# Optimization experiments

Hardware: AMD Instinct MI355X
Metric: run time of the kernel (lower is better)

## Reference

```python
import jax, jax.numpy as jnp
import numpy as np

NUM_GRAPHS = 64
EPS = 1e-5


def _bn(x, g, b):
    # training-mode BatchNorm1d with biased variance (as torch uses for normalization)
    m = x.mean(axis=0)
    v = x.var(axis=0)
    return (x - m) * jax.lax.rsqrt(v + EPS) * g + b


def setup_inputs() -> dict:
    key = jax.random.key(0)
    ks = jax.random.split(key, 16)
    N, E, F, T, H = 50000, 500000, 8, 8, 64
    d = {
        "x": jax.random.normal(ks[0], (N, F), jnp.float32),
        "edge_index": jax.random.randint(ks[1], (2, E), 0, N),
        "edge_attr": jax.random.uniform(ks[2], (E, T), jnp.float32),
        "batch_index": jnp.sort(jax.random.randint(ks[3], (N,), 0, NUM_GRAPHS)),
        # edge_nn: Linear(T,16) -> ReLU -> Linear(16, F*H)
        "w_e1": jax.random.normal(ks[4], (T, 16), jnp.float32) * 0.2,
        "b_e1": jnp.zeros((16,), jnp.float32),
        "w_e2": jax.random.normal(ks[5], (16, F * H), jnp.float32) * 0.1,
        "b_e2": jnp.zeros((F * H,), jnp.float32),
        # NNConv root weight + bias
        "root": jax.random.normal(ks[6], (F, H), jnp.float32) * 0.2,
        "conv_bias": jnp.zeros((H,), jnp.float32),
        "g_bnc": jnp.ones((H,), jnp.float32), "b_bnc": jnp.zeros((H,), jnp.float32),
        "w1": jax.random.normal(ks[7], (2 * H, 256), jnp.float32) * 0.08,
        "b1": jnp.zeros((256,), jnp.float32),
        "g1": jnp.ones((256,), jnp.float32), "be1": jnp.zeros((256,), jnp.float32),
        "w2": jax.random.normal(ks[8], (256, 128), jnp.float32) * 0.08,
        "b2": jnp.zeros((128,), jnp.float32),
        "g2": jnp.ones((128,), jnp.float32), "be2": jnp.zeros((128,), jnp.float32),
        "w3": jax.random.normal(ks[9], (128, 64), jnp.float32) * 0.1,
        "b3": jnp.zeros((64,), jnp.float32),
        "g3": jnp.ones((64,), jnp.float32), "be3": jnp.zeros((64,), jnp.float32),
        "wout": jax.random.normal(ks[10], (64, 10), jnp.float32) * 0.1,
        "bout": jnp.zeros((10,), jnp.float32),
    }
    return d


def reference(x, edge_index, edge_attr, batch_index,
              w_e1, b_e1, w_e2, b_e2, root, conv_bias, g_bnc, b_bnc,
              w1, b1, g1, be1, w2, b2, g2, be2, w3, b3, g3, be3, wout, bout):
    N, F = x.shape
    H = root.shape[1]
    src, dst = edge_index[0], edge_index[1]

    # edge-conditioned weights: edge_nn(edge_attr) -> [E, F, H]
    h_e = jax.nn.relu(edge_attr @ w_e1 + b_e1)
    W_e = (h_e @ w_e2 + b_e2).reshape(-1, F, H)

    # gather source features, per-edge matmul, scatter-mean into targets
    msg = jnp.einsum('ef,efh->eh', x[src], W_e)            # [E, H]
    agg = jax.ops.segment_sum(msg, dst, num_segments=N)
    deg = jax.ops.segment_sum(jnp.ones((msg.shape[0],), msg.dtype), dst, num_segments=N)
    agg = agg / jnp.maximum(deg, 1.0)[:, None]
    h = x @ root + agg + conv_bias                          # NNConv output [N, H]

    h = jax.nn.relu(_bn(h, g_bnc, b_bnc))

    # global mean + max pooling per graph
    gs = jax.ops.segment_sum(h, batch_index, num_segments=NUM_GRAPHS)
    cnt = jax.ops.segment_sum(jnp.ones((N,), h.dtype), batch_index, num_segments=NUM_GRAPHS)
    gmean = gs / jnp.maximum(cnt, 1.0)[:, None]
    gmax = jax.ops.segment_max(h, batch_index, num_segments=NUM_GRAPHS)
    gmax = jnp.where(cnt[:, None] > 0, gmax, 0.0)
    g = jnp.concatenate([gmean, gmax], axis=1)              # [G, 2H]

    g = jax.nn.relu(_bn(g @ w1 + b1, g1, be1))
    g = jax.nn.relu(_bn(g @ w2 + b2, g2, be2))
    g = jax.nn.relu(_bn(g @ w3 + b3, g3, be3))
    return g @ wout + bout
```

## Files before the change

### kernel.cpp

```cpp
#include <hip/hip_runtime.h>

#define DEG_CAP 64
#define ZROW 144
#define ZPAD 148

__device__ __forceinline__ int rfl(int v) { return __builtin_amdgcn_readfirstlane(v); }

__global__ void k_he(const float* __restrict__ ea, const float* __restrict__ w,
                     const float* __restrict__ b, float* __restrict__ he, int E) {
  int e = blockIdx.x * blockDim.x + threadIdx.x;
  if (e >= E) return;
  const float4* eap = reinterpret_cast<const float4*>(ea + (size_t)e * 8);
  float4 a0 = eap[0], a1 = eap[1];
  float av[8] = {a0.x, a0.y, a0.z, a0.w, a1.x, a1.y, a1.z, a1.w};
  float o[16];
#pragma unroll
  for (int k = 0; k < 16; ++k) o[k] = b[k];
#pragma unroll
  for (int t = 0; t < 8; ++t) {
    float at = av[t];
#pragma unroll
    for (int k = 0; k < 16; ++k) o[k] = fmaf(at, w[t * 16 + k], o[k]);
  }
#pragma unroll
  for (int k = 0; k < 16; ++k) o[k] = fmaxf(o[k], 0.f);
  float4* hp = reinterpret_cast<float4*>(he + (size_t)e * 16);
  hp[0] = make_float4(o[0], o[1], o[2], o[3]);
  hp[1] = make_float4(o[4], o[5], o[6], o[7]);
  hp[2] = make_float4(o[8], o[9], o[10], o[11]);
  hp[3] = make_float4(o[12], o[13], o[14], o[15]);
}

__global__ void k_fill(const int* __restrict__ ei, int* __restrict__ cursor,
                       int* __restrict__ slots, int E) {
  int e = blockIdx.x * blockDim.x + threadIdx.x;
  if (e >= E) return;
  int dst = ei[E + e];
  int slot = atomicAdd(&cursor[dst], 1);
  if (slot < DEG_CAP) slots[(size_t)dst * DEG_CAP + slot] = e;
}

__global__ void k_zgather(const float* __restrict__ x, const int* __restrict__ ei,
                          const float* __restrict__ he, const int* __restrict__ cursor,
                          const int* __restrict__ slots, float* __restrict__ zbuf,
                          int N) {
  int lane = threadIdx.x & 63;
  int n = rfl(blockIdx.x * (blockDim.x >> 6) + (threadIdx.x >> 6));
  if (n >= N) return;
  int k = lane >> 2;
  int f2 = (lane & 3) << 1;
  int d = cursor[n];
  int dc = min(d, DEG_CAP);
  int eid = (lane < dc) ? slots[(size_t)n * DEG_CAP + lane] : 0;
  int sid = ei[eid];
  float z0 = 0.f, z1 = 0.f, xs0 = 0.f, xs1 = 0.f;
  if (dc > 0) {
    int e0 = __shfl(eid, 0), s0 = __shfl(sid, 0);
    float hk = he[(size_t)e0 * 16 + k];
    float2 xv = *reinterpret_cast<const float2*>(x + (size_t)s0 * 8 + f2);
    for (int i = 1; i < dc; ++i) {
      int e1 = __shfl(eid, i), s1 = __shfl(sid, i);
      float hk_n = he[(size_t)e1 * 16 + k];
      float2 xv_n = *reinterpret_cast<const float2*>(x + (size_t)s1 * 8 + f2);
      z0 = fmaf(hk, xv.x, z0);
      z1 = fmaf(hk, xv.y, z1);
      xs0 += xv.x; xs1 += xv.y;
      hk = hk_n; xv = xv_n;
    }
    z0 = fmaf(hk, xv.x, z0);
    z1 = fmaf(hk, xv.y, z1);
    xs0 += xv.x; xs1 += xv.y;
  }
  float inv = 1.f / (float)max(d, 1);
  z0 *= inv; z1 *= inv; xs0 *= inv; xs1 *= inv;
  float2* zp = reinterpret_cast<float2*>(zbuf + (size_t)n * ZROW);
  zp[lane] = make_float2(z0, z1);
  if (lane < 4) zp[64 + lane] = make_float2(xs0, xs1);
  if (lane < 8) zbuf[(size_t)n * ZROW + 136 + lane] = x[(size_t)n * 8 + lane];
}

__global__ __launch_bounds__(256) void k_zwgemm(
    const float* __restrict__ zbuf, const float* __restrict__ w_e2,
    const float* __restrict__ b_e2, const float* __restrict__ root,
    const float* __restrict__ conv_bias, float* __restrict__ hout,
    float* __restrict__ stats, int N) {
  __shared__ float wt[ZROW * 64];
  __shared__ float zt[64 * ZPAD];
  __shared__ float sl[128];
  int t = threadIdx.x;
  int n0 = blockIdx.x * 64;

  for (int i = t; i < ZROW * 64; i += 256) {
    int j = i >> 6, hh = i & 63;
    float v;
    if (j < 128) {
      int k = j >> 3, f = (((j >> 1) & 3) << 1) | (j & 1);
      v = w_e2[k * 512 + f * 64 + hh];
    } else if (j < 136) {
      v = b_e2[(j - 128) * 64 + hh];
    } else {
      v = root[(j - 136) * 64 + hh];
    }
    wt[i] = v;
  }
  for (int i4 = t; i4 < 64 * ZROW / 4; i4 += 256) {
    int dw = i4 << 2;
    int r = dw / ZROW;
    int c = dw - r * ZROW;
    float4 v = make_float4(0.f, 0.f, 0.f, 0.f);
    if (n0 + r < N)
      v = *reinterpret_cast<const float4*>(zbuf + (size_t)(n0 + r) * ZROW + c);
    *reinterpret_cast<float4*>(&zt[r * ZPAD + c]) = v;
  }
  if (t < 128) sl[t] = 0.f;
  __syncthreads();

  int hg = t & 15;
  int ng = t >> 4;
  float acc[4][4];
#pragma unroll
  for (int i = 0; i < 4; ++i)
#pragma unroll
    for (int q = 0; q < 4; ++q) acc[i][q] = 0.f;

  for (int j = 0; j < ZROW; j += 4) {
    float za[4][4], wa[4][4];
#pragma unroll
    for (int i = 0; i < 4; ++i) {
      float4 v = *reinterpret_cast<const float4*>(&zt[(ng * 4 + i) * ZPAD + j]);
      za[i][0] = v.x; za[i][1] = v.y; za[i][2] = v.z; za[i][3] = v.w;
    }
#pragma unroll
    for (int r = 0; r < 4; ++r) {
      float4 v = *reinterpret_cast<const float4*>(&wt[(j + r) * 64 + hg * 4]);
      wa[r][0] = v.x; wa[r][1] = v.y; wa[r][2] = v.z; wa[r][3] = v.w;
    }
#pragma unroll
    for (int r = 0; r < 4; ++r)
#pragma unroll
      for (int i = 0; i < 4; ++i)
#pragma unroll
        for (int q = 0; q < 4; ++q)
          acc[i][q] = fmaf(za[i][r], wa[r][q], acc[i][q]);
  }

  float cb[4];
#pragma unroll
  for (int q = 0; q < 4; ++q) cb[q] = conv_bias[hg * 4 + q];
  float bns[4] = {0.f, 0.f, 0.f, 0.f}, bnq[4] = {0.f, 0.f, 0.f, 0.f};
#pragma unroll
  for (int i = 0; i < 4; ++i) {
    int n = n0 + ng * 4 + i;
    float h0 = acc[i][0] + cb[0], h1 = acc[i][1] + cb[1];
    float h2 = acc[i][2] + cb[2], h3 = acc[i][3] + cb[3];
    if (n < N) {
      *reinterpret_cast<float4*>(&hout[(size_t)n * 64 + hg * 4]) =
          make_float4(h0, h1, h2, h3);
      bns[0] += h0; bns[1] += h1; bns[2] += h2; bns[3] += h3;
      bnq[0] += h0 * h0; bnq[1] += h1 * h1; bnq[2] += h2 * h2; bnq[3] += h3 * h3;
    }
  }
#pragma unroll
  for (int q = 0; q < 4; ++q) {
    bns[q] += __shfl_xor(bns[q], 16); bns[q] += __shfl_xor(bns[q], 32);
    bnq[q] += __shfl_xor(bnq[q], 16); bnq[q] += __shfl_xor(bnq[q], 32);
  }
  if ((t & 48) == 0) {
#pragma unroll
    for (int q = 0; q < 4; ++q) {
      atomicAdd(&sl[hg * 4 + q], bns[q]);
      atomicAdd(&sl[64 + hg * 4 + q], bnq[q]);
    }
  }
  __syncthreads();
  if (t < 128) atomicAdd(&stats[t], sl[t]);
}

__global__ void k_bnpool(const float* __restrict__ hbuf, const float* __restrict__ stats,
                         const int* __restrict__ batch, const float* __restrict__ gamma,
                         const float* __restrict__ beta, float* __restrict__ gsum,
                         unsigned int* __restrict__ gmax, int* __restrict__ gcnt, int N) {
  int lane = threadIdx.x & 63;
  int wid = blockIdx.x * (blockDim.x >> 6) + (threadIdx.x >> 6);
  int nw = gridDim.x * (blockDim.x >> 6);
  float m = stats[lane] / (float)N;
  float var = stats[64 + lane] / (float)N - m * m;
  float rs = rsqrtf(var + 1e-5f);
  float ga = gamma[lane], be = beta[lane];
  int per = (N + nw - 1) / nw;
  int n0 = wid * per;
  int n1 = min(N, n0 + per);
  int cur = -1, cnt = 0;
  float s = 0.f, mx = 0.f;
  for (int n = n0; n < n1; ++n) {
    int g = batch[n];
    float v = hbuf[(size_t)n * 64 + lane];
    float y = fmaxf(fmaf((v - m) * rs, ga, be), 0.f);
    if (g != cur) {
      if (cur >= 0) {
        atomicAdd(&gsum[cur * 64 + lane], s);
        atomicMax(&gmax[cur * 64 + lane], __float_as_uint(mx));
        if (lane == 0) atomicAdd(&gcnt[cur], cnt);
      }
      cur = g; s = 0.f; mx = 0.f; cnt = 0;
    }
    s += y; mx = fmaxf(mx, y); ++cnt;
  }
  if (cur >= 0) {
    atomicAdd(&gsum[cur * 64 + lane], s);
    atomicMax(&gmax[cur * 64 + lane], __float_as_uint(mx));
    if (lane == 0) atomicAdd(&gcnt[cur], cnt);
  }
}

__global__ void k_head_pool(const float* __restrict__ gsum,
                            const unsigned int* __restrict__ gmax,
                            const int* __restrict__ gcnt,
                            const float* __restrict__ W, const float* __restrict__ b,
                            const float* __restrict__ gamma, const float* __restrict__ beta,
                            float* __restrict__ out, int Kout) {
  int lane = threadIdx.x & 63;
  int col = blockIdx.x * (blockDim.x >> 6) + (threadIdx.x >> 6);
  if (col >= Kout) return;
  float inv = 1.f / fmaxf((float)gcnt[lane], 1.f);
  float a = b[col];
#pragma unroll 4
  for (int k = 0; k < 64; ++k)
    a = fmaf(gsum[lane * 64 + k] * inv, W[(size_t)k * Kout + col], a);
#pragma unroll 4
  for (int k = 0; k < 64; ++k)
    a = fmaf(__uint_as_float(gmax[lane * 64 + k]), W[(size_t)(64 + k) * Kout + col], a);
  float sv = a, ss = a * a;
#pragma unroll
  for (int off = 32; off > 0; off >>= 1) {
    sv += __shfl_xor(sv, off);
    ss += __shfl_xor(ss, off);
  }
  float m = sv * (1.f / 64.f);
  float var = ss * (1.f / 64.f) - m * m;
  float y = fmaxf(fmaf((a - m) * rsqrtf(var + 1e-5f), gamma[col], beta[col]), 0.f);
  out[(size_t)lane * Kout + col] = y;
}

__global__ void k_head(const float* __restrict__ in, const float* __restrict__ W,
                       const float* __restrict__ b, const float* __restrict__ gamma,
                       const float* __restrict__ beta, float* __restrict__ out,
                       int Kin, int Kout) {
  int lane = threadIdx.x & 63;
  int col = blockIdx.x * (blockDim.x >> 6) + (threadIdx.x >> 6);
  if (col >= Kout) return;
  const float4* ir = reinterpret_cast<const float4*>(in + (size_t)lane * Kin);
  float a = b[col];
  for (int k4 = 0; k4 < (Kin >> 2); ++k4) {
    float4 v = ir[k4];
    int k = k4 << 2;
    a = fmaf(v.x, W[(size_t)k * Kout + col], a);
    a = fmaf(v.y, W[(size_t)(k + 1) * Kout + col], a);
    a = fmaf(v.z, W[(size_t)(k + 2) * Kout + col], a);
    a = fmaf(v.w, W[(size_t)(k + 3) * Kout + col], a);
  }
  float sv = a, ss = a * a;
#pragma unroll
  for (int off = 32; off > 0; off >>= 1) {
    sv += __shfl_xor(sv, off);
    ss += __shfl_xor(ss, off);
  }
  float m = sv * (1.f / 64.f);
  float var = ss * (1.f / 64.f) - m * m;
  float y = fmaxf(fmaf((a - m) * rsqrtf(var + 1e-5f), gamma[col], beta[col]), 0.f);
  out[(size_t)lane * Kout + col] = y;
}

__global__ void k_out(const float* __restrict__ in, const float* __restrict__ W,
                      const float* __restrict__ b, float* __restrict__ out) {
  int t = threadIdx.x;
  if (t >= 640) return;
  int r = t / 10, c = t % 10;
  float a = b[c];
#pragma unroll
  for (int k = 0; k < 64; ++k) a = fmaf(in[r * 64 + k], W[k * 10 + c], a);
  out[t] = a;
}

extern "C" void kernel_launch(void* const* d_in, const int* in_sizes, int n_in,
                              void* d_out, int out_size, void* d_ws, size_t ws_size,
                              hipStream_t stream) {
  const float* x = (const float*)d_in[0];
  const int* ei = (const int*)d_in[1];
  const float* ea = (const float*)d_in[2];
  const int* batch = (const int*)d_in[3];
  const float* w_e1 = (const float*)d_in[4];
  const float* b_e1 = (const float*)d_in[5];
  const float* w_e2 = (const float*)d_in[6];
  const float* b_e2 = (const float*)d_in[7];
  const float* root = (const float*)d_in[8];
  const float* conv_bias = (const float*)d_in[9];
  const float* g_bnc = (const float*)d_in[10];
  const float* b_bnc = (const float*)d_in[11];
  const float* w1 = (const float*)d_in[12];
  const float* b1 = (const float*)d_in[13];
  const float* g1 = (const float*)d_in[14];
  const float* be1 = (const float*)d_in[15];
  const float* w2 = (const float*)d_in[16];
  const float* b2 = (const float*)d_in[17];
  const float* g2 = (const float*)d_in[18];
  const float* be2 = (const float*)d_in[19];
  const float* w3 = (const float*)d_in[20];
  const float* b3 = (const float*)d_in[21];
  const float* g3 = (const float*)d_in[22];
  const float* be3 = (const float*)d_in[23];
  const float* wout = (const float*)d_in[24];
  const float* bout = (const float*)d_in[25];

  int N = in_sizes[0] / 8;
  int E = in_sizes[1] / 2;

  char* wsb = (char*)d_ws;
  size_t off = 0;
  auto alloc = [&](size_t bytes) -> void* {
    void* p = wsb + off;
    off += (bytes + 255) & ~(size_t)255;
    return p;
  };
  float* he = (float*)alloc((size_t)E * 16 * 4);
  int* cursor = (int*)alloc((size_t)N * 4);
  int* slots = (int*)alloc((size_t)N * DEG_CAP * 4);
  float* zbuf = (float*)alloc((size_t)N * ZROW * 4);
  float* hbuf = (float*)alloc((size_t)N * 64 * 4);
  float* zblk = (float*)alloc(8384 * 4);
  float* stats = zblk;
  float* gsum = zblk + 128;
  unsigned int* gmax = (unsigned int*)(zblk + 128 + 4096);
  int* gcnt = (int*)(zblk + 128 + 8192);
  float* l1 = (float*)alloc(64 * 256 * 4);
  float* l2 = (float*)alloc(64 * 128 * 4);
  float* l3 = (float*)alloc(64 * 64 * 4);

  hipMemsetAsync(cursor, 0, (size_t)N * 4, stream);
  hipMemsetAsync(zblk, 0, 8384 * 4, stream);

  const int tb = 256;
  k_he<<<(E + tb - 1) / tb, tb, 0, stream>>>(ea, w_e1, b_e1, he, E);
  k_fill<<<(E + tb - 1) / tb, tb, 0, stream>>>(ei, cursor, slots, E);
  k_zgather<<<(N + 3) / 4, 256, 0, stream>>>(x, ei, he, cursor, slots, zbuf, N);
  k_zwgemm<<<(N + 63) / 64, 256, 0, stream>>>(zbuf, w_e2, b_e2, root, conv_bias,
                                              hbuf, stats, N);
  k_bnpool<<<512, 256, 0, stream>>>(hbuf, stats, batch, g_bnc, b_bnc, gsum, gmax, gcnt, N);
  k_head_pool<<<64, 256, 0, stream>>>(gsum, gmax, gcnt, w1, b1, g1, be1, l1, 256);
  k_head<<<32, 256, 0, stream>>>(l1, w2, b2, g2, be2, l2, 256, 128);
  k_head<<<16, 256, 0, stream>>>(l2, w3, b3, g3, be3, l3, 128, 64);
  k_out<<<1, 640, 0, stream>>>(l3, wout, bout, (float*)d_out);
}
```

Baseline: 308.7 us.

## Fuse edge MLP into gather, precompute weight table, merge MLP head into one kernel

Removes the separate per-edge hidden-layer kernel and its E×16 buffer by recomputing the ReLU(edge_attr@w_e1) value inside the gather loop, and stores the source index next to the edge id in the slot list. The weight-matrix permutation moves into the fill kernel so the GEMM reads it from global/L1 instead of rebuilding it in LDS per block, which also frees LDS. The four small head kernels merge into a single 1024-thread block kernel, and the two memsets become one. The cost is redundant edge-MLP arithmetic and wider slot storage, with GEMM weight reads now going through cache instead of shared memory.

```diff
diff --git a/kernel.cpp b/kernel.cpp
--- a/kernel.cpp
+++ b/kernel.cpp
@@ -6,69 +6,75 @@
 
 __device__ __forceinline__ int rfl(int v) { return __builtin_amdgcn_readfirstlane(v); }
 
-__global__ void k_he(const float* __restrict__ ea, const float* __restrict__ w,
-                     const float* __restrict__ b, float* __restrict__ he, int E) {
+__global__ void k_fill(const int* __restrict__ ei, const float* __restrict__ w_e2,
+                       const float* __restrict__ b_e2, const float* __restrict__ root,
+                       int* __restrict__ cursor, int2* __restrict__ slots2,
+                       float* __restrict__ wlin, int E) {
   int e = blockIdx.x * blockDim.x + threadIdx.x;
-  if (e >= E) return;
-  const float4* eap = reinterpret_cast<const float4*>(ea + (size_t)e * 8);
-  float4 a0 = eap[0], a1 = eap[1];
-  float av[8] = {a0.x, a0.y, a0.z, a0.w, a1.x, a1.y, a1.z, a1.w};
-  float o[16];
-#pragma unroll
-  for (int k = 0; k < 16; ++k) o[k] = b[k];
-#pragma unroll
-  for (int t = 0; t < 8; ++t) {
-    float at = av[t];
-#pragma unroll
-    for (int k = 0; k < 16; ++k) o[k] = fmaf(at, w[t * 16 + k], o[k]);
-  }
-#pragma unroll
-  for (int k = 0; k < 16; ++k) o[k] = fmaxf(o[k], 0.f);
-  float4* hp = reinterpret_cast<float4*>(he + (size_t)e * 16);
-  hp[0] = make_float4(o[0], o[1], o[2], o[3]);
-  hp[1] = make_float4(o[4], o[5], o[6], o[7]);
-  hp[2] = make_float4(o[8], o[9], o[10], o[11]);
-  hp[3] = make_float4(o[12], o[13], o[14], o[15]);
-}
-
-__global__ void k_fill(const int* __restrict__ ei, int* __restrict__ cursor,
-                       int* __restrict__ slots, int E) {
-  int e = blockIdx.x * blockDim.x + threadIdx.x;
+  if (e < ZROW * 64) {
+    int j = e >> 6, h = e & 63;
+    float v;
+    if (j < 128) {
+      int k = j >> 3, f = (((j >> 1) & 3) << 1) | (j & 1);
+      v = w_e2[k * 512 + f * 64 + h];
+    } else if (j < 136) {
+      v = b_e2[(j - 128) * 64 + h];
+    } else {
+      v = root[(j - 136) * 64 + h];
+    }
+    wlin[e] = v;
+  }
   if (e >= E) return;
   int dst = ei[E + e];
+  int src = ei[e];
   int slot = atomicAdd(&cursor[dst], 1);
-  if (slot < DEG_CAP) slots[(size_t)dst * DEG_CAP + slot] = e;
-}
-
-__global__ void k_zgather(const float* __restrict__ x, const int* __restrict__ ei,
-                          const float* __restrict__ he, const int* __restrict__ cursor,
-                          const int* __restrict__ slots, float* __restrict__ zbuf,
-                          int N) {
+  if (slot < DEG_CAP) slots2[(size_t)dst * DEG_CAP + slot] = make_int2(e, src);
+}
+
+__global__ void k_zgather(const float* __restrict__ x, const float* __restrict__ ea,
+                          const float* __restrict__ w_e1, const float* __restrict__ b_e1,
+                          const int* __restrict__ cursor, const int2* __restrict__ slots2,
+                          float* __restrict__ zbuf, int N) {
   int lane = threadIdx.x & 63;
   int n = rfl(blockIdx.x * (blockDim.x >> 6) + (threadIdx.x >> 6));
   if (n >= N) return;
   int k = lane >> 2;
   int f2 = (lane & 3) << 1;
+  float w1c[8];
+#pragma unroll
+  for (int t = 0; t < 8; ++t) w1c[t] = w_e1[t * 16 + k];
+  float bk = b_e1[k];
   int d = cursor[n];
   int dc = min(d, DEG_CAP);
-  int eid = (lane < dc) ? slots[(size_t)n * DEG_CAP + lane] : 0;
-  int sid = ei[eid];
+  int2 sl = (lane < dc) ? slots2[(size_t)n * DEG_CAP + lane] : make_int2(0, 0);
   float z0 = 0.f, z1 = 0.f, xs0 = 0.f, xs1 = 0.f;
   if (dc > 0) {
-    int e0 = __shfl(eid, 0), s0 = __shfl(sid, 0);
-    float hk = he[(size_t)e0 * 16 + k];
+    int e0 = __shfl(sl.x, 0), s0 = __shfl(sl.y, 0);
+    float4 a0 = *reinterpret_cast<const float4*>(ea + (size_t)e0 * 8);
+    float4 a1 = *reinterpret_cast<const float4*>(ea + (size_t)e0 * 8 + 4);
     float2 xv = *reinterpret_cast<const float2*>(x + (size_t)s0 * 8 + f2);
     for (int i = 1; i < dc; ++i) {
-      int e1 = __shfl(eid, i), s1 = __shfl(sid, i);
-      float hk_n = he[(size_t)e1 * 16 + k];
-      float2 xv_n = *reinterpret_cast<const float2*>(x + (size_t)s1 * 8 + f2);
-      z0 = fmaf(hk, xv.x, z0);
-      z1 = fmaf(hk, xv.y, z1);
+      int e1 = __shfl(sl.x, i), s1 = __shfl(sl.y, i);
+      float4 n0 = *reinterpret_cast<const float4*>(ea + (size_t)e1 * 8);
+      float4 n1 = *reinterpret_cast<const float4*>(ea + (size_t)e1 * 8 + 4);
+      float2 xn = *reinterpret_cast<const float2*>(x + (size_t)s1 * 8 + f2);
+      float he = bk;
+      he = fmaf(a0.x, w1c[0], he); he = fmaf(a0.y, w1c[1], he);
+      he = fmaf(a0.z, w1c[2], he); he = fmaf(a0.w, w1c[3], he);
+      he = fmaf(a1.x, w1c[4], he); he = fmaf(a1.y, w1c[5], he);
+      he = fmaf(a1.z, w1c[6], he); he = fmaf(a1.w, w1c[7], he);
+      he = fmaxf(he, 0.f);
+      z0 = fmaf(he, xv.x, z0); z1 = fmaf(he, xv.y, z1);
       xs0 += xv.x; xs1 += xv.y;
-      hk = hk_n; xv = xv_n;
-    }
-    z0 = fmaf(hk, xv.x, z0);
-    z1 = fmaf(hk, xv.y, z1);
+      a0 = n0; a1 = n1; xv = xn;
+    }
+    float he = bk;
+    he = fmaf(a0.x, w1c[0], he); he = fmaf(a0.y, w1c[1], he);
+    he = fmaf(a0.z, w1c[2], he); he = fmaf(a0.w, w1c[3], he);
+    he = fmaf(a1.x, w1c[4], he); he = fmaf(a1.y, w1c[5], he);
+    he = fmaf(a1.z, w1c[6], he); he = fmaf(a1.w, w1c[7], he);
+    he = fmaxf(he, 0.f);
+    z0 = fmaf(he, xv.x, z0); z1 = fmaf(he, xv.y, z1);
     xs0 += xv.x; xs1 += xv.y;
   }
   float inv = 1.f / (float)max(d, 1);
@@ -80,29 +86,14 @@
 }
 
 __global__ __launch_bounds__(256) void k_zwgemm(
-    const float* __restrict__ zbuf, const float* __restrict__ w_e2,
-    const float* __restrict__ b_e2, const float* __restrict__ root,
+    const float* __restrict__ zbuf, const float* __restrict__ wlin,
     const float* __restrict__ conv_bias, float* __restrict__ hout,
     float* __restrict__ stats, int N) {
-  __shared__ float wt[ZROW * 64];
   __shared__ float zt[64 * ZPAD];
   __shared__ float sl[128];
   int t = threadIdx.x;
   int n0 = blockIdx.x * 64;
 
-  for (int i = t; i < ZROW * 64; i += 256) {
-    int j = i >> 6, hh = i & 63;
-    float v;
-    if (j < 128) {
-      int k = j >> 3, f = (((j >> 1) & 3) << 1) | (j & 1);
-      v = w_e2[k * 512 + f * 64 + hh];
-    } else if (j < 136) {
-      v = b_e2[(j - 128) * 64 + hh];
-    } else {
-      v = root[(j - 136) * 64 + hh];
-    }
-    wt[i] = v;
-  }
   for (int i4 = t; i4 < 64 * ZROW / 4; i4 += 256) {
     int dw = i4 << 2;
     int r = dw / ZROW;
@@ -124,24 +115,33 @@
     for (int q = 0; q < 4; ++q) acc[i][q] = 0.f;
 
   for (int j = 0; j < ZROW; j += 4) {
-    float za[4][4], wa[4][4];
+    float4 wv[4];
+#pragma unroll
+    for (int r = 0; r < 4; ++r)
+      wv[r] = *reinterpret_cast<const float4*>(&wlin[(j + r) * 64 + hg * 4]);
+    float4 zv[4];
+#pragma unroll
+    for (int i = 0; i < 4; ++i)
+      zv[i] = *reinterpret_cast<const float4*>(&zt[(ng * 4 + i) * ZPAD + j]);
 #pragma unroll
     for (int i = 0; i < 4; ++i) {
-      float4 v = *reinterpret_cast<const float4*>(&zt[(ng * 4 + i) * ZPAD + j]);
-      za[i][0] = v.x; za[i][1] = v.y; za[i][2] = v.z; za[i][3] = v.w;
-    }
-#pragma unroll
-    for (int r = 0; r < 4; ++r) {
-      float4 v = *reinterpret_cast<const float4*>(&wt[(j + r) * 64 + hg * 4]);
-      wa[r][0] = v.x; wa[r][1] = v.y; wa[r][2] = v.z; wa[r][3] = v.w;
-    }
-#pragma unroll
-    for (int r = 0; r < 4; ++r)
-#pragma unroll
-      for (int i = 0; i < 4; ++i)
-#pragma unroll
-        for (int q = 0; q < 4; ++q)
-          acc[i][q] = fmaf(za[i][r], wa[r][q], acc[i][q]);
+      acc[i][0] = fmaf(zv[i].x, wv[0].x, acc[i][0]);
+      acc[i][1] = fmaf(zv[i].x, wv[0].y, acc[i][1]);
+      acc[i][2] = fmaf(zv[i].x, wv[0].z, acc[i][2]);
+      acc[i][3] = fmaf(zv[i].x, wv[0].w, acc[i][3]);
+      acc[i][0] = fmaf(zv[i].y, wv[1].x, acc[i][0]);
+      acc[i][1] = fmaf(zv[i].y, wv[1].y, acc[i][1]);
+      acc[i][2] = fmaf(zv[i].y, wv[1].z, acc[i][2]);
+      acc[i][3] = fmaf(zv[i].y, wv[1].w, acc[i][3]);
+      acc[i][0] = fmaf(zv[i].z, wv[2].x, acc[i][0]);
+      acc[i][1] = fmaf(zv[i].z, wv[2].y, acc[i][1]);
+      acc[i][2] = fmaf(zv[i].z, wv[2].z, acc[i][2]);
+      acc[i][3] = fmaf(zv[i].z, wv[2].w, acc[i][3]);
+      acc[i][0] = fmaf(zv[i].w, wv[3].x, acc[i][0]);
+      acc[i][1] = fmaf(zv[i].w, wv[3].y, acc[i][1]);
+      acc[i][2] = fmaf(zv[i].w, wv[3].z, acc[i][2]);
+      acc[i][3] = fmaf(zv[i].w, wv[3].w, acc[i][3]);
+    }
   }
 
   float cb[4];
@@ -213,73 +213,135 @@
   }
 }
 
-__global__ void k_head_pool(const float* __restrict__ gsum,
-                            const unsigned int* __restrict__ gmax,
-                            const int* __restrict__ gcnt,
-                            const float* __restrict__ W, const float* __restrict__ b,
-                            const float* __restrict__ gamma, const float* __restrict__ beta,
-                            float* __restrict__ out, int Kout) {
-  int lane = threadIdx.x & 63;
-  int col = blockIdx.x * (blockDim.x >> 6) + (threadIdx.x >> 6);
-  if (col >= Kout) return;
-  float inv = 1.f / fmaxf((float)gcnt[lane], 1.f);
-  float a = b[col];
-#pragma unroll 4
-  for (int k = 0; k < 64; ++k)
-    a = fmaf(gsum[lane * 64 + k] * inv, W[(size_t)k * Kout + col], a);
-#pragma unroll 4
-  for (int k = 0; k < 64; ++k)
-    a = fmaf(__uint_as_float(gmax[lane * 64 + k]), W[(size_t)(64 + k) * Kout + col], a);
-  float sv = a, ss = a * a;
-#pragma unroll
-  for (int off = 32; off > 0; off >>= 1) {
-    sv += __shfl_xor(sv, off);
-    ss += __shfl_xor(ss, off);
-  }
-  float m = sv * (1.f / 64.f);
-  float var = ss * (1.f / 64.f) - m * m;
-  float y = fmaxf(fmaf((a - m) * rsqrtf(var + 1e-5f), gamma[col], beta[col]), 0.f);
-  out[(size_t)lane * Kout + col] = y;
-}
-
-__global__ void k_head(const float* __restrict__ in, const float* __restrict__ W,
-                       const float* __restrict__ b, const float* __restrict__ gamma,
-                       const float* __restrict__ beta, float* __restrict__ out,
-                       int Kin, int Kout) {
-  int lane = threadIdx.x & 63;
-  int col = blockIdx.x * (blockDim.x >> 6) + (threadIdx.x >> 6);
-  if (col >= Kout) return;
-  const float4* ir = reinterpret_cast<const float4*>(in + (size_t)lane * Kin);
-  float a = b[col];
-  for (int k4 = 0; k4 < (Kin >> 2); ++k4) {
-    float4 v = ir[k4];
-    int k = k4 << 2;
-    a = fmaf(v.x, W[(size_t)k * Kout + col], a);
-    a = fmaf(v.y, W[(size_t)(k + 1) * Kout + col], a);
-    a = fmaf(v.z, W[(size_t)(k + 2) * Kout + col], a);
-    a = fmaf(v.w, W[(size_t)(k + 3) * Kout + col], a);
-  }
-  float sv = a, ss = a * a;
-#pragma unroll
-  for (int off = 32; off > 0; off >>= 1) {
-    sv += __shfl_xor(sv, off);
-    ss += __shfl_xor(ss, off);
-  }
-  float m = sv * (1.f / 64.f);
-  float var = ss * (1.f / 64.f) - m * m;
-  float y = fmaxf(fmaf((a - m) * rsqrtf(var + 1e-5f), gamma[col], beta[col]), 0.f);
-  out[(size_t)lane * Kout + col] = y;
-}
-
-__global__ void k_out(const float* __restrict__ in, const float* __restrict__ W,
-                      const float* __restrict__ b, float* __restrict__ out) {
+#define PA 132
+#define PB 260
+__global__ __launch_bounds__(1024) void k_mlphead(
+    const float* __restrict__ gsum, const unsigned int* __restrict__ gmaxu,
+    const int* __restrict__ gcnt,
+    const float* __restrict__ W1, const float* __restrict__ B1,
+    const float* __restrict__ G1, const float* __restrict__ E1,
+    const float* __restrict__ W2, const float* __restrict__ B2,
+    const float* __restrict__ G2, const float* __restrict__ E2,
+    const float* __restrict__ W3, const float* __restrict__ B3,
+    const float* __restrict__ G3, const float* __restrict__ E3,
+    const float* __restrict__ Wo, const float* __restrict__ Bo,
+    float* __restrict__ out) {
+  __shared__ float A[64 * PA];
+  __shared__ float B[64 * PB];
   int t = threadIdx.x;
-  if (t >= 640) return;
-  int r = t / 10, c = t % 10;
-  float a = b[c];
-#pragma unroll
-  for (int k = 0; k < 64; ++k) a = fmaf(in[r * 64 + k], W[k * 10 + c], a);
-  out[t] = a;
+
+  for (int i = t; i < 64 * 128; i += 1024) {
+    int r = i >> 7, c = i & 127;
+    float v;
+    if (c < 64) v = gsum[r * 64 + c] / fmaxf((float)gcnt[r], 1.f);
+    else v = __uint_as_float(gmaxu[r * 64 + (c - 64)]);
+    A[r * PA + c] = v;
+  }
+  __syncthreads();
+
+  {
+    int c = t & 255, rg = t >> 8;
+    float acc[16];
+    float bb = B1[c];
+#pragma unroll
+    for (int i = 0; i < 16; ++i) acc[i] = bb;
+    for (int k = 0; k < 128; k += 4) {
+      float w0 = W1[(k + 0) * 256 + c], w1 = W1[(k + 1) * 256 + c];
+      float w2 = W1[(k + 2) * 256 + c], w3 = W1[(k + 3) * 256 + c];
+#pragma unroll
+      for (int i = 0; i < 16; ++i) {
+        float4 gv = *reinterpret_cast<const float4*>(&A[(rg * 16 + i) * PA + k]);
+        acc[i] = fmaf(gv.x, w0, acc[i]); acc[i] = fmaf(gv.y, w1, acc[i]);
+        acc[i] = fmaf(gv.z, w2, acc[i]); acc[i] = fmaf(gv.w, w3, acc[i]);
+      }
+    }
+#pragma unroll
+    for (int i = 0; i < 16; ++i) B[(rg * 16 + i) * PB + c] = acc[i];
+  }
+  __syncthreads();
+  if (t < 256) {
+    float s = 0.f, q = 0.f;
+    for (int r = 0; r < 64; ++r) { float v = B[r * PB + t]; s += v; q += v * v; }
+    float m = s * (1.f / 64.f), var = q * (1.f / 64.f) - m * m;
+    float rs = rsqrtf(var + 1e-5f), ga = G1[t], be = E1[t];
+    for (int r = 0; r < 64; ++r) {
+      float v = B[r * PB + t];
+      B[r * PB + t] = fmaxf(fmaf((v - m) * rs, ga, be), 0.f);
+    }
+  }
+  __syncthreads();
+
+  {
+    int c = t & 127, rg = t >> 7;
+    float acc[8];
+    float bb = B2[c];
+#pragma unroll
+    for (int i = 0; i < 8; ++i) acc[i] = bb;
+    for (int k = 0; k < 256; k += 4) {
+      float w0 = W2[(k + 0) * 128 + c], w1 = W2[(k + 1) * 128 + c];
+      float w2 = W2[(k + 2) * 128 + c], w3 = W2[(k + 3) * 128 + c];
+#pragma unroll
+      for (int i = 0; i < 8; ++i) {
+        float4 v = *reinterpret_cast<const float4*>(&B[(rg * 8 + i) * PB + k]);
+        acc[i] = fmaf(v.x, w0, acc[i]); acc[i] = fmaf(v.y, w1, acc[i]);
+        acc[i] = fmaf(v.z, w2, acc[i]); acc[i] = fmaf(v.w, w3, acc[i]);
+      }
+    }
+#pragma unroll
+    for (int i = 0; i < 8; ++i) A[(rg * 8 + i) * PA + c] = acc[i];
+  }
+  __syncthreads();
+  if (t < 128) {
+    float s = 0.f, q = 0.f;
+    for (int r = 0; r < 64; ++r) { float v = A[r * PA + t]; s += v; q += v * v; }
+    float m = s * (1.f / 64.f), var = q * (1.f / 64.f) - m * m;
+    float rs = rsqrtf(var + 1e-5f), ga = G2[t], be = E2[t];
+    for (int r = 0; r < 64; ++r) {
+      float v = A[r * PA + t];
+      A[r * PA + t] = fmaxf(fmaf((v - m) * rs, ga, be), 0.f);
+    }
+  }
+  __syncthreads();
+
+  {
+    int c = t & 63, rg = t >> 6;
+    float acc[4];
+    float bb = B3[c];
+#pragma unroll
+    for (int i = 0; i < 4; ++i) acc[i] = bb;
+    for (int k = 0; k < 128; k += 4) {
+      float w0 = W3[(k + 0) * 64 + c], w1 = W3[(k + 1) * 64 + c];
+      float w2 = W3[(k + 2) * 64 + c], w3 = W3[(k + 3) * 64 + c];
+#pragma unroll
+      for (int i = 0; i < 4; ++i) {
+        float4 v = *reinterpret_cast<const float4*>(&A[(rg * 4 + i) * PA + k]);
+        acc[i] = fmaf(v.x, w0, acc[i]); acc[i] = fmaf(v.y, w1, acc[i]);
+        acc[i] = fmaf(v.z, w2, acc[i]); acc[i] = fmaf(v.w, w3, acc[i]);
+      }
+    }
+#pragma unroll
+    for (int i = 0; i < 4; ++i) B[(rg * 4 + i) * PB + c] = acc[i];
+  }
+  __syncthreads();
+  if (t < 64) {
+    float s = 0.f, q = 0.f;
+    for (int r = 0; r < 64; ++r) { float v = B[r * PB + t]; s += v; q += v * v; }
+    float m = s * (1.f / 64.f), var = q * (1.f / 64.f) - m * m;
+    float rs = rsqrtf(var + 1e-5f), ga = G3[t], be = E3[t];
+    for (int r = 0; r < 64; ++r) {
+      float v = B[r * PB + t];
+      B[r * PB + t] = fmaxf(fmaf((v - m) * rs, ga, be), 0.f);
+    }
+  }
+  __syncthreads();
+
+  if (t < 640) {
+    int r = t / 10, c = t - r * 10;
+    float a = Bo[c];
+#pragma unroll
+    for (int k = 0; k < 64; ++k) a = fmaf(B[r * PB + k], Wo[k * 10 + c], a);
+    out[r * 10 + c] = a;
+  }
 }
 
 extern "C" void kernel_launch(void* const* d_in, const int* in_sizes, int n_in,
@@ -322,32 +384,28 @@
     off += (bytes + 255) & ~(size_t)255;
     return p;
   };
-  float* he = (float*)alloc((size_t)E * 16 * 4);
-  int* cursor = (int*)alloc((size_t)N * 4);
-  int* slots = (int*)alloc((size_t)N * DEG_CAP * 4);
-  float* zbuf = (float*)alloc((size_t)N * ZROW * 4);
-  float* hbuf = (float*)alloc((size_t)N * 64 * 4);
-  float* zblk = (float*)alloc(8384 * 4);
+  size_t zeroBytes = (size_t)N * 4 + 8384 * 4;
+  int* cursor = (int*)alloc(zeroBytes);
+  float* zblk = (float*)((char*)cursor + (size_t)N * 4);
   float* stats = zblk;
   float* gsum = zblk + 128;
   unsigned int* gmax = (unsigned int*)(zblk + 128 + 4096);
   int* gcnt = (int*)(zblk + 128 + 8192);
-  float* l1 = (float*)alloc(64 * 256 * 4);
-  float* l2 = (float*)alloc(64 * 128 * 4);
-  float* l3 = (float*)alloc(64 * 64 * 4);
-
-  hipMemsetAsync(cursor, 0, (size_t)N * 4, stream);
-  hipMemsetAsync(zblk, 0, 8384 * 4, stream);
+  int2* slots2 = (int2*)alloc((size_t)N * DEG_CAP * 8);
+  float* wlin = (float*)alloc(ZROW * 64 * 4);
+  float* zbuf = (float*)alloc((size_t)N * ZROW * 4);
+  float* hbuf = (float*)alloc((size_t)N * 64 * 4);
+
+  hipMemsetAsync(cursor, 0, zeroBytes, stream);
 
   const int tb = 256;
-  k_he<<<(E + tb - 1) / tb, tb, 0, stream>>>(ea, w_e1, b_e1, he, E);
-  k_fill<<<(E + tb - 1) / tb, tb, 0, stream>>>(ei, cursor, slots, E);
-  k_zgather<<<(N + 3) / 4, 256, 0, stream>>>(x, ei, he, cursor, slots, zbuf, N);
-  k_zwgemm<<<(N + 63) / 64, 256, 0, stream>>>(zbuf, w_e2, b_e2, root, conv_bias,
-                                              hbuf, stats, N);
+  k_fill<<<(E + tb - 1) / tb, tb, 0, stream>>>(ei, w_e2, b_e2, root, cursor,
+                                               slots2, wlin, E);
+  k_zgather<<<(N + 3) / 4, 256, 0, stream>>>(x, ea, w_e1, b_e1, cursor, slots2,
+                                             zbuf, N);
+  k_zwgemm<<<(N + 63) / 64, 256, 0, stream>>>(zbuf, wlin, conv_bias, hbuf, stats, N);
   k_bnpool<<<512, 256, 0, stream>>>(hbuf, stats, batch, g_bnc, b_bnc, gsum, gmax, gcnt, N);
-  k_head_pool<<<64, 256, 0, stream>>>(gsum, gmax, gcnt, w1, b1, g1, be1, l1, 256);
-  k_head<<<32, 256, 0, stream>>>(l1, w2, b2, g2, be2, l2, 256, 128);
-  k_head<<<16, 256, 0, stream>>>(l2, w3, b3, g3, be3, l3, 128, 64);
-  k_out<<<1, 640, 0, stream>>>(l3, wout, bout, (float*)d_out);
-}
+  k_mlphead<<<1, 1024, 0, stream>>>(gsum, gmax, gcnt,
+                                    w1, b1, g1, be1, w2, b2, g2, be2,
+                                    w3, b3, g3, be3, wout, bout, (float*)d_out);
+}
```

Measured after the change: 313.5 us. About the same (+1.6%).
